# Optimization experiments

Measured on AMD Instinct MI355X. Metric: run time of the kernel, lower is better.

Reference implementation:

```python
import jax, jax.numpy as jnp
import numpy as np

B, D, C, N = 256, 512, 345, 50000
K = 5
ALPHA = 1.0
EPS = 1e-12


def setup_inputs() -> dict:
    key = jax.random.key(0)
    k1, k2, k3, k4, k5 = jax.random.split(key, 5)
    return {
        "features": jax.random.normal(k1, (B, D), dtype=jnp.float32),
        "predictions": jax.random.normal(k2, (B, C), dtype=jnp.float32),
        "fea_bank": jax.random.normal(k3, (N, D), dtype=jnp.float32),
        "score_bank": jax.random.uniform(k4, (N, C), dtype=jnp.float32, minval=1e-3, maxval=1.0),
        "trg_idx": jax.random.randint(k5, (B,), 0, N, dtype=jnp.int64),
    }


def reference(features, predictions, fea_bank, score_bank, trg_idx):
    softmax_out = jax.nn.softmax(predictions, axis=1)  # [B, C]

    # --- no_grad block: bank update + neighbor retrieval ---
    f_norm = features / jnp.maximum(
        jnp.linalg.norm(features, axis=1, keepdims=True), EPS
    )
    f_ng = jax.lax.stop_gradient(f_norm)
    s_ng = jax.lax.stop_gradient(softmax_out)
    fb = fea_bank.at[trg_idx].set(f_ng)       # [N, D]
    sb = score_bank.at[trg_idx].set(s_ng)     # [N, C]
    distance = f_ng @ fb.T                    # [B, N] cosine similarity
    _, idx_near = jax.lax.top_k(distance, K + 1)
    idx_near = idx_near[:, 1:]                # drop self -> [B, K]
    score_near = sb[idx_near]                 # [B, K, C]

    # F.kl_div(input=softmax_out (NOT log), target=score_near):
    # target * (log(target) - input), summed over C and K, mean over B.
    kl = score_near * (jnp.log(score_near) - softmax_out[:, None, :])
    loss = jnp.mean(kl.sum(-1).sum(-1))

    # dispersion: masked pairwise dot of softmax outputs (off-diagonal)
    dot = softmax_out @ softmax_out.T         # [B, B]
    mask = 1.0 - jnp.eye(B, dtype=dot.dtype)
    neg_pred = jnp.mean((dot * mask).sum(-1))
    loss = loss + ALPHA * neg_pred
    return loss
```

## Files before the change

kernel.cpp:

```cpp
#include <hip/hip_runtime.h>
#include <cstdint>

#define BB 256
#define DD 512
#define CC 345
#define NBANK 50000
#define NPAD 50048
#define KNEI 5
#define ALPHAC 1.0f
#define EPSN 1e-12f
#define NHALF 782
#define CSLOTS (NHALF * 2)

typedef short short8 __attribute__((ext_vector_type(8)));
typedef float f32x4 __attribute__((ext_vector_type(4)));
typedef unsigned long long u64;

__device__ inline uint32_t f2bf1(float x) {
    union { float f; uint32_t u; } v; v.f = x;
    return (v.u + 0x7FFFu + ((v.u >> 16) & 1u)) >> 16;
}
__device__ inline uint32_t pack2(float a, float b) {
    return f2bf1(a) | (f2bf1(b) << 16);
}
__device__ inline float bl(uint32_t x) {
    union { uint32_t u; float f; } v; v.u = x << 16; return v.f;
}
__device__ inline float bh(uint32_t x) {
    union { uint32_t u; float f; } v; v.u = x & 0xFFFF0000u; return v.f;
}
__device__ inline u64 mkkey(float v, int j) {
    union { float f; uint32_t u; } c; c.f = v;
    uint32_t b = c.u;
    uint32_t k = (b & 0x80000000u) ? ~b : (b | 0x80000000u);
    return ((u64)k << 32) | (uint32_t)(~j);
}
__device__ inline u64 umax64(u64 a, u64 b) { return a > b ? a : b; }
__device__ inline u64 shfl_xor_u64(u64 v, int m) {
    int lo = __shfl_xor((int)(uint32_t)v, m, 64);
    int hi = __shfl_xor((int)(v >> 32), m, 64);
    return ((u64)(uint32_t)hi << 32) | (uint32_t)lo;
}
__device__ inline void ins6u(u64 k, u64* lv) {
    if (k > lv[5]) {
        int q = 5;
        while (q > 0 && k > lv[q - 1]) { lv[q] = lv[q - 1]; q--; }
        lv[q] = k;
    }
}
__device__ inline void tree6u(u64* sv, int t, const u64* lv) {
#pragma unroll
    for (int r = 0; r < 6; r++) sv[t * 6 + r] = lv[r];
    __syncthreads();
    for (int s = 128; s > 0; s >>= 1) {
        if (t < s) {
            u64 av[6], bv[6], rv[6];
#pragma unroll
            for (int r = 0; r < 6; r++) { av[r] = sv[t * 6 + r]; bv[r] = sv[(t + s) * 6 + r]; }
            int x = 0, y = 0;
#pragma unroll
            for (int o = 0; o < 6; o++) {
                bool pk = av[x] > bv[y];
                rv[o] = pk ? av[x] : bv[y];
                x += pk; y += !pk;
            }
#pragma unroll
            for (int r = 0; r < 6; r++) sv[t * 6 + r] = rv[r];
        }
        __syncthreads();
    }
}
__device__ inline void async16(const void* g, void* l) {
    __builtin_amdgcn_global_load_lds(
        (const __attribute__((address_space(1))) unsigned int*)g,
        (__attribute__((address_space(3))) unsigned int*)l, 16, 0, 0);
}
__device__ inline size_t sw_off(int tile, int r, int ch) {
    return (size_t)tile * 8192 + r * 64 + ((ch ^ (r & 7)) * 8);
}

__global__ void repl_init_kernel(int* __restrict__ repl) {
    int idx = blockIdx.x * 256 + threadIdx.x;
    if (idx < NPAD) repl[idx] = -1;
}

__global__ void winner_kernel(const int* __restrict__ trg, int* __restrict__ repl,
                              float* __restrict__ out) {
    int t = threadIdx.x;
    __shared__ int st[BB];
    if (t == 0) out[0] = 0.f;
    st[t] = trg[t];
    __syncthreads();
    int mv = st[t];
    int w = 1;
    for (int b2 = t + 1; b2 < BB; b2++)
        if (st[b2] == mv) w = 0;
    if (w) repl[mv] = t;
}

__global__ void norm_softmax_kernel(const float* __restrict__ feat,
                                    const float* __restrict__ pred,
                                    unsigned short* __restrict__ fnb,
                                    unsigned short* __restrict__ fnb2,
                                    float* __restrict__ p) {
    int b = blockIdx.x, t = threadIdx.x;
    __shared__ float red[256];
    float x0 = feat[b * DD + t];
    float x1 = feat[b * DD + t + 256];
    red[t] = x0 * x0 + x1 * x1;
    __syncthreads();
    for (int s = 128; s > 0; s >>= 1) {
        if (t < s) red[t] += red[t + s];
        __syncthreads();
    }
    float inv = 1.0f / fmaxf(sqrtf(red[0]), EPSN);
    if (t < 64) {
        const f32x4* src = (const f32x4*)(feat + b * DD + t * 8);
        f32x4 f0 = src[0], f1 = src[1];
        uint4 u = make_uint4(pack2(f0[0] * inv, f0[1] * inv),
                             pack2(f0[2] * inv, f0[3] * inv),
                             pack2(f1[0] * inv, f1[1] * inv),
                             pack2(f1[2] * inv, f1[3] * inv));
        *(uint4*)(fnb + b * DD + t * 8) = u;
        int mtile = b >> 7, r = b & 127, kt = t >> 3, ch = t & 7;
        *(uint4*)(fnb2 + sw_off(mtile * 8 + kt, r, ch)) = u;
    }
    __syncthreads();
    float y0 = (t < CC) ? pred[b * CC + t] : -3.0e38f;
    float y1 = (t + 256 < CC) ? pred[b * CC + t + 256] : -3.0e38f;
    red[t] = fmaxf(y0, y1);
    __syncthreads();
    for (int s = 128; s > 0; s >>= 1) {
        if (t < s) red[t] = fmaxf(red[t], red[t + s]);
        __syncthreads();
    }
    float M = red[0];
    __syncthreads();
    float e0 = (t < CC) ? expf(y0 - M) : 0.f;
    float e1 = (t + 256 < CC) ? expf(y1 - M) : 0.f;
    red[t] = e0 + e1;
    __syncthreads();
    for (int s = 128; s > 0; s >>= 1) {
        if (t < s) red[t] += red[t + s];
        __syncthreads();
    }
    float si = 1.0f / red[0];
    if (t < CC) p[b * CC + t] = e0 * si;
    if (t + 256 < CC) p[b * CC + t + 256] = e1 * si;
}

__global__ __launch_bounds__(256) void gemm_topk_kernel(
        const unsigned short* __restrict__ fnb2, const float* __restrict__ bank,
        const unsigned short* __restrict__ fnb, const int* __restrict__ repl,
        u64* __restrict__ cand) {
    __shared__ __align__(16) char smem[40960];
    unsigned short* As = (unsigned short*)smem;
    unsigned short* Bs = (unsigned short*)(smem + 32768);

    int t = threadIdx.x;
    int ntb = blockIdx.x;
    int j0 = ntb * 64;
    int w = t >> 6, lane = t & 63, quad = lane >> 4, l16 = lane & 15;

    int br = t >> 2, cq = t & 3;
    int bj = j0 + br;
    int rp = (bj < NBANK) ? repl[bj] : -2;

    f32x4 acc[4][4];
#pragma unroll
    for (int mt = 0; mt < 4; mt++)
#pragma unroll
        for (int nt = 0; nt < 4; nt++)
            acc[mt][nt] = (f32x4){0.f, 0.f, 0.f, 0.f};

    const char* fnb2b = (const char*)fnb2;

    for (int kt = 0; kt < 8; kt++) {
        const char* asrc = fnb2b + (size_t)((w < 2 ? kt : kt + 8) * 16384 + (w & 1) * 8192);
        char* adst = smem + w * 8192;
#pragma unroll
        for (int u = 0; u < 8; u++)
            async16(asrc + u * 1024 + lane * 16, adst + u * 1024);
        {
            uint4 b0, b1;
            if (rp >= 0) {
                const uint4* s = (const uint4*)(fnb + (size_t)rp * DD + kt * 64 + cq * 16);
                b0 = s[0]; b1 = s[1];
            } else if (rp == -1) {
                const f32x4* s = (const f32x4*)(bank + (size_t)bj * DD + kt * 64 + cq * 16);
                f32x4 f0 = s[0], f1 = s[1], f2 = s[2], f3 = s[3];
                b0 = make_uint4(pack2(f0[0], f0[1]), pack2(f0[2], f0[3]),
                                pack2(f1[0], f1[1]), pack2(f1[2], f1[3]));
                b1 = make_uint4(pack2(f2[0], f2[1]), pack2(f2[2], f2[3]),
                                pack2(f3[0], f3[1]), pack2(f3[2], f3[3]));
            } else {
                b0 = make_uint4(0, 0, 0, 0);
                b1 = make_uint4(0, 0, 0, 0);
            }
            int c0 = cq * 2;
            *(uint4*)(Bs + br * 64 + ((c0 ^ (br & 7)) * 8)) = b0;
            *(uint4*)(Bs + br * 64 + (((c0 + 1) ^ (br & 7)) * 8)) = b1;
        }
        __syncthreads();
#pragma unroll
        for (int ks = 0; ks < 2; ks++) {
            int swz = ((ks * 4 + quad) ^ (l16 & 7)) * 8;
            short8 af[4], bf[4];
#pragma unroll
            for (int mt = 0; mt < 4; mt++)
                af[mt] = *(const short8*)(As + (w * 64 + mt * 16 + l16) * 64 + swz);
#pragma unroll
            for (int nt = 0; nt < 4; nt++)
                bf[nt] = *(const short8*)(Bs + (nt * 16 + l16) * 64 + swz);
#pragma unroll
            for (int mt = 0; mt < 4; mt++)
#pragma unroll
                for (int nt = 0; nt < 4; nt++)
                    acc[mt][nt] = __builtin_amdgcn_mfma_f32_16x16x32_bf16(
                        af[mt], bf[nt], acc[mt][nt], 0, 0, 0);
        }
        __syncthreads();
    }

    bool maskPad[4];
#pragma unroll
    for (int nt = 0; nt < 4; nt++)
        maskPad[nt] = (ntb == NHALF - 1) && ((j0 + nt * 16 + l16) >= NBANK);

#pragma unroll
    for (int mt = 0; mt < 4; mt++)
#pragma unroll
        for (int r2 = 0; r2 < 4; r2++) {
            u64 k[4];
#pragma unroll
            for (int nt = 0; nt < 4; nt++) {
                int j = j0 + nt * 16 + l16;
                k[nt] = maskPad[nt] ? 0ull : mkkey(acc[mt][nt][r2], j);
            }
            u64 m = umax64(umax64(k[0], k[1]), umax64(k[2], k[3]));
#pragma unroll
            for (int off = 1; off < 16; off <<= 1)
                m = umax64(m, shfl_xor_u64(m, off));
            u64 top1 = m;
#pragma unroll
            for (int nt = 0; nt < 4; nt++) k[nt] = (k[nt] == top1) ? 0ull : k[nt];
            m = umax64(umax64(k[0], k[1]), umax64(k[2], k[3]));
#pragma unroll
            for (int off = 1; off < 16; off <<= 1)
                m = umax64(m, shfl_xor_u64(m, off));
            if (l16 == 0) {
                int gi = w * 64 + mt * 16 + quad * 4 + r2;
                u64* cp = cand + (size_t)gi * CSLOTS + ntb * 2;
                cp[0] = top1; cp[1] = m;
            }
        }
}

__global__ __launch_bounds__(256) void merge_kernel(
        const u64* __restrict__ cand, const unsigned short* __restrict__ fnb,
        const float* __restrict__ bank, const int* __restrict__ repl,
        int* __restrict__ nidx) {
    int i = blockIdx.x, t = threadIdx.x;
    __shared__ u64 sv[1536];
    __shared__ uint32_t fm[25];
    __shared__ int fl[128];
    __shared__ int nf;
    __shared__ float a[512];
    const u64* cr = cand + (size_t)i * CSLOTS;

    u64 lv[6] = {0, 0, 0, 0, 0, 0};
    for (int q = t; q < CSLOTS; q += 256) ins6u(cr[q], lv);
    if (t < 25) fm[t] = 0;
    if (t == 0) nf = 0;
    tree6u(sv, t, lv);
    u64 M6 = sv[5];
    __syncthreads();
    for (int h = t; h < NHALF; h += 256) {
        if (cr[h * 2 + 1] >= M6) {
            int s = atomicAdd(&nf, 1);
            if (s < 128) fl[s] = h;
            atomicOr(&fm[h >> 5], 1u << (h & 31));
        }
    }
    __syncthreads();
    if (nf > 0) {
        uint32_t wrd = ((const uint32_t*)(fnb + (size_t)i * DD))[t];
        a[2 * t] = bl(wrd);
        a[2 * t + 1] = bh(wrd);
        __syncthreads();
        u64 l2[6] = {0, 0, 0, 0, 0, 0};
        for (int q = t; q < CSLOTS; q += 256) {
            int h = q >> 1;
            if (!((fm[h >> 5] >> (h & 31)) & 1u)) ins6u(cr[q], l2);
        }
        int nfl = nf < 128 ? nf : 128;
        for (int s = 0; s < nfl; s++) {
            int h = fl[s];
            if (t < 64) {
                int j = h * 64 + t;
                if (j < NBANK) {
                    int rp = repl[j];
                    float dot = 0.f;
                    if (rp >= 0) {
                        const uint32_t* rw = (const uint32_t*)(fnb + (size_t)rp * DD);
                        for (int kk = 0; kk < 256; kk++) {
                            uint32_t u = rw[kk];
                            dot += bl(u) * a[2 * kk] + bh(u) * a[2 * kk + 1];
                        }
                    } else {
                        const float* rw = bank + (size_t)j * DD;
                        for (int kk = 0; kk < DD; kk++)
                            dot += bl(f2bf1(rw[kk])) * a[kk];
                    }
                    ins6u(mkkey(dot, j), l2);
                }
            }
        }
        __syncthreads();
        tree6u(sv, t, l2);
    }
    if (t == 0) {
#pragma unroll
        for (int r = 1; r < 6; r++)
            nidx[i * KNEI + r - 1] = (int)(~(uint32_t)(sv[r] & 0xFFFFFFFFull));
    }
}

__global__ void kl_negpred_kernel(const float* __restrict__ p,
                                  const float* __restrict__ sbank,
                                  const int* __restrict__ nidx,
                                  const int* __restrict__ trg,
                                  float* __restrict__ out) {
    int bid = blockIdx.x, t = threadIdx.x;
    __shared__ float red[256];
    __shared__ float aux[256];
    if (bid < BB) {
        int b = bid;
        __shared__ int st[BB];
        __shared__ int sj[KNEI], sb[KNEI];
        st[t] = trg[t];
        __syncthreads();
        if (t < KNEI) {
            int j = nidx[b * KNEI + t];
            sj[t] = j;
            int src = -1;
            for (int b2 = 0; b2 < BB; b2++)
                if (st[b2] == j) src = b2;
            sb[t] = src;
        }
        __syncthreads();
        float local = 0.f;
        for (int k = 0; k < KNEI; k++) {
            int j = sj[k], src = sb[k];
            const float* srow = (src >= 0) ? (p + src * CC) : (sbank + (size_t)j * CC);
            for (int c = t; c < CC; c += 256) {
                float s = srow[c];
                local += s * (logf(s) - p[b * CC + c]);
            }
        }
        red[t] = local;
        __syncthreads();
        for (int s = 128; s > 0; s >>= 1) {
            if (t < s) red[t] += red[t + s];
            __syncthreads();
        }
        if (t == 0) atomicAdd(out, red[0] * (1.0f / BB));
    } else {
        int c = bid - BB;
        float v = p[t * CC + c];
        red[t] = v;
        aux[t] = v * v;
        __syncthreads();
        for (int s = 128; s > 0; s >>= 1) {
            if (t < s) { red[t] += red[t + s]; aux[t] += aux[t + s]; }
            __syncthreads();
        }
        if (t == 0) atomicAdd(out, ALPHAC * (red[0] * red[0] - aux[0]) * (1.0f / BB));
    }
}

extern "C" void kernel_launch(void* const* d_in, const int* in_sizes, int n_in,
                              void* d_out, int out_size, void* d_ws, size_t ws_size,
                              hipStream_t stream) {
    const float* feat  = (const float*)d_in[0];
    const float* pred  = (const float*)d_in[1];
    const float* bank  = (const float*)d_in[2];
    const float* sbank = (const float*)d_in[3];
    const int*   trg   = (const int*)d_in[4];
    float* out = (float*)d_out;

    char* ws = (char*)d_ws;
    unsigned short* fnb2 = (unsigned short*)ws;
    unsigned short* fnb  = (unsigned short*)(ws + 262144);
    float*          p    = (float*)(ws + 524288);
    int*            repl = (int*)(ws + 877568);
    u64*            cand = (u64*)(ws + 1077760);
    int*            nidx = (int*)(ws + 4280832);

    repl_init_kernel<<<(NPAD + 255) / 256, 256, 0, stream>>>(repl);
    winner_kernel<<<1, 256, 0, stream>>>(trg, repl, out);
    norm_softmax_kernel<<<BB, 256, 0, stream>>>(feat, pred, fnb, fnb2, p);
    gemm_topk_kernel<<<NHALF, 256, 0, stream>>>(fnb2, bank, fnb, repl, cand);
    merge_kernel<<<BB, 256, 0, stream>>>(cand, fnb, bank, repl, nidx);
    kl_negpred_kernel<<<BB + CC, 256, 0, stream>>>(p, sbank, nidx, trg, out);
}
```

Baseline: 278.5 us.

## Double-buffer LDS tiles and prefetch bank rows in GEMM-topk kernel

Splits shared memory into two stages in the similarity GEMM kernel. The next K-slice's A tile is copied asynchronously and the next bank row is loaded into registers while MFMAs run on the current slice. The B tile is converted and stored after compute, which removes one barrier per iteration and hides global load latency. The cost is doubled LDS per block (about 80KB), which may cut the number of resident blocks per CU, plus extra registers for the prefetched data.

```diff
diff --git a/kernel.cpp b/kernel.cpp
--- a/kernel.cpp
+++ b/kernel.cpp
@@ -153,9 +153,7 @@
         const unsigned short* __restrict__ fnb2, const float* __restrict__ bank,
         const unsigned short* __restrict__ fnb, const int* __restrict__ repl,
         u64* __restrict__ cand) {
-    __shared__ __align__(16) char smem[40960];
-    unsigned short* As = (unsigned short*)smem;
-    unsigned short* Bs = (unsigned short*)(smem + 32768);
+    __shared__ __align__(16) char smem[2][40960];
 
     int t = threadIdx.x;
     int ntb = blockIdx.x;
@@ -165,6 +163,9 @@
     int br = t >> 2, cq = t & 3;
     int bj = j0 + br;
     int rp = (bj < NBANK) ? repl[bj] : -2;
+    const uint4* fsrc = (const uint4*)(fnb + (size_t)((rp >= 0) ? rp : 0) * DD) + cq * 2;
+    const f32x4* bsrc = (const f32x4*)(bank + (size_t)bj * DD) + cq * 4;
+    const char* fnb2b = (const char*)fnb2;
 
     f32x4 acc[4][4];
 #pragma unroll
@@ -173,35 +174,50 @@
         for (int nt = 0; nt < 4; nt++)
             acc[mt][nt] = (f32x4){0.f, 0.f, 0.f, 0.f};
 
-    const char* fnb2b = (const char*)fnb2;
-
-    for (int kt = 0; kt < 8; kt++) {
-        const char* asrc = fnb2b + (size_t)((w < 2 ? kt : kt + 8) * 16384 + (w & 1) * 8192);
-        char* adst = smem + w * 8192;
+    uint4 pb0, pb1;
+    f32x4 pf0, pf1, pf2, pf3;
+
+    if (rp >= 0)       { pb0 = fsrc[0]; pb1 = fsrc[1]; }
+    else if (rp == -1) { pf0 = bsrc[0]; pf1 = bsrc[1]; pf2 = bsrc[2]; pf3 = bsrc[3]; }
+    {
+        const char* asrc = fnb2b + (size_t)((w < 2 ? 0 : 8) * 16384 + (w & 1) * 8192);
+        char* adst = smem[0] + w * 8192;
 #pragma unroll
         for (int u = 0; u < 8; u++)
             async16(asrc + u * 1024 + lane * 16, adst + u * 1024);
-        {
-            uint4 b0, b1;
-            if (rp >= 0) {
-                const uint4* s = (const uint4*)(fnb + (size_t)rp * DD + kt * 64 + cq * 16);
-                b0 = s[0]; b1 = s[1];
-            } else if (rp == -1) {
-                const f32x4* s = (const f32x4*)(bank + (size_t)bj * DD + kt * 64 + cq * 16);
-                f32x4 f0 = s[0], f1 = s[1], f2 = s[2], f3 = s[3];
-                b0 = make_uint4(pack2(f0[0], f0[1]), pack2(f0[2], f0[3]),
-                                pack2(f1[0], f1[1]), pack2(f1[2], f1[3]));
-                b1 = make_uint4(pack2(f2[0], f2[1]), pack2(f2[2], f2[3]),
-                                pack2(f3[0], f3[1]), pack2(f3[2], f3[3]));
-            } else {
-                b0 = make_uint4(0, 0, 0, 0);
-                b1 = make_uint4(0, 0, 0, 0);
-            }
-            int c0 = cq * 2;
-            *(uint4*)(Bs + br * 64 + ((c0 ^ (br & 7)) * 8)) = b0;
-            *(uint4*)(Bs + br * 64 + (((c0 + 1) ^ (br & 7)) * 8)) = b1;
-        }
-        __syncthreads();
+    }
+    {
+        uint4 b0, b1;
+        if (rp >= 0)       { b0 = pb0; b1 = pb1; }
+        else if (rp == -1) {
+            b0 = make_uint4(pack2(pf0[0], pf0[1]), pack2(pf0[2], pf0[3]),
+                            pack2(pf1[0], pf1[1]), pack2(pf1[2], pf1[3]));
+            b1 = make_uint4(pack2(pf2[0], pf2[1]), pack2(pf2[2], pf2[3]),
+                            pack2(pf3[0], pf3[1]), pack2(pf3[2], pf3[3]));
+        } else { b0 = make_uint4(0, 0, 0, 0); b1 = make_uint4(0, 0, 0, 0); }
+        unsigned short* Bs0 = (unsigned short*)(smem[0] + 32768);
+        int c0 = cq * 2;
+        *(uint4*)(Bs0 + br * 64 + ((c0 ^ (br & 7)) * 8)) = b0;
+        *(uint4*)(Bs0 + br * 64 + (((c0 + 1) ^ (br & 7)) * 8)) = b1;
+    }
+    __syncthreads();
+
+    for (int kt = 0; kt < 8; kt++) {
+        int cur = kt & 1;
+        int nxt = cur ^ 1;
+        if (kt < 7) {
+            if (rp >= 0)       { pb0 = fsrc[(kt + 1) * 8];  pb1 = fsrc[(kt + 1) * 8 + 1]; }
+            else if (rp == -1) { pf0 = bsrc[(kt + 1) * 16];     pf1 = bsrc[(kt + 1) * 16 + 1];
+                                 pf2 = bsrc[(kt + 1) * 16 + 2]; pf3 = bsrc[(kt + 1) * 16 + 3]; }
+            const char* asrc = fnb2b +
+                (size_t)((w < 2 ? kt + 1 : kt + 9) * 16384 + (w & 1) * 8192);
+            char* adst = smem[nxt] + w * 8192;
+#pragma unroll
+            for (int u = 0; u < 8; u++)
+                async16(asrc + u * 1024 + lane * 16, adst + u * 1024);
+        }
+        unsigned short* As = (unsigned short*)smem[cur];
+        unsigned short* Bs = (unsigned short*)(smem[cur] + 32768);
 #pragma unroll
         for (int ks = 0; ks < 2; ks++) {
             int swz = ((ks * 4 + quad) ^ (l16 & 7)) * 8;
@@ -218,6 +234,20 @@
                 for (int nt = 0; nt < 4; nt++)
                     acc[mt][nt] = __builtin_amdgcn_mfma_f32_16x16x32_bf16(
                         af[mt], bf[nt], acc[mt][nt], 0, 0, 0);
+        }
+        if (kt < 7) {
+            uint4 b0, b1;
+            if (rp >= 0)       { b0 = pb0; b1 = pb1; }
+            else if (rp == -1) {
+                b0 = make_uint4(pack2(pf0[0], pf0[1]), pack2(pf0[2], pf0[3]),
+                                pack2(pf1[0], pf1[1]), pack2(pf1[2], pf1[3]));
+                b1 = make_uint4(pack2(pf2[0], pf2[1]), pack2(pf2[2], pf2[3]),
+                                pack2(pf3[0], pf3[1]), pack2(pf3[2], pf3[3]));
+            } else { b0 = make_uint4(0, 0, 0, 0); b1 = make_uint4(0, 0, 0, 0); }
+            unsigned short* Bn = (unsigned short*)(smem[nxt] + 32768);
+            int c0 = cq * 2;
+            *(uint4*)(Bn + br * 64 + ((c0 ^ (br & 7)) * 8)) = b0;
+            *(uint4*)(Bn + br * 64 + (((c0 + 1) ^ (br & 7)) * 8)) = b1;
         }
         __syncthreads();
     }
```

Result: no change. 279.8 us (+0.5%).

## Stage whole bank tile in LDS once, read A from global, fuse small kernels

Applied to the files above, without the earlier changes.

The GEMM/top-k kernel now loads the full 64-row bank tile (all 512 dims, converted to bf16 and swizzled) into 64KB of LDS up front. It then runs the MFMA loop without per-k-step barriers, reading the query fragments directly from the global normalized-feature buffer instead of async-copying a pre-swizzled A layout into LDS. The repl init is folded into the norm/softmax kernel, and the merge kernel is fused with the KL and dispersion reduction, which drops the extra pre-swizzled buffer and two launches. The larger LDS footprint lowers occupancy, and A reads now depend on L1/L2 hits.

```diff
diff --git a/kernel.cpp b/kernel.cpp
--- a/kernel.cpp
+++ b/kernel.cpp
@@ -70,40 +70,15 @@
         __syncthreads();
     }
 }
-__device__ inline void async16(const void* g, void* l) {
-    __builtin_amdgcn_global_load_lds(
-        (const __attribute__((address_space(1))) unsigned int*)g,
-        (__attribute__((address_space(3))) unsigned int*)l, 16, 0, 0);
-}
-__device__ inline size_t sw_off(int tile, int r, int ch) {
-    return (size_t)tile * 8192 + r * 64 + ((ch ^ (r & 7)) * 8);
-}
-
-__global__ void repl_init_kernel(int* __restrict__ repl) {
-    int idx = blockIdx.x * 256 + threadIdx.x;
-    if (idx < NPAD) repl[idx] = -1;
-}
-
-__global__ void winner_kernel(const int* __restrict__ trg, int* __restrict__ repl,
-                              float* __restrict__ out) {
-    int t = threadIdx.x;
-    __shared__ int st[BB];
-    if (t == 0) out[0] = 0.f;
-    st[t] = trg[t];
-    __syncthreads();
-    int mv = st[t];
-    int w = 1;
-    for (int b2 = t + 1; b2 < BB; b2++)
-        if (st[b2] == mv) w = 0;
-    if (w) repl[mv] = t;
-}
 
 __global__ void norm_softmax_kernel(const float* __restrict__ feat,
                                     const float* __restrict__ pred,
                                     unsigned short* __restrict__ fnb,
-                                    unsigned short* __restrict__ fnb2,
-                                    float* __restrict__ p) {
+                                    float* __restrict__ p,
+                                    int* __restrict__ repl) {
     int b = blockIdx.x, t = threadIdx.x;
+    int gi = b * 256 + t;
+    if (gi < NPAD) repl[gi] = -1;
     __shared__ float red[256];
     float x0 = feat[b * DD + t];
     float x1 = feat[b * DD + t + 256];
@@ -122,8 +97,6 @@
                              pack2(f1[0] * inv, f1[1] * inv),
                              pack2(f1[2] * inv, f1[3] * inv));
         *(uint4*)(fnb + b * DD + t * 8) = u;
-        int mtile = b >> 7, r = b & 127, kt = t >> 3, ch = t & 7;
-        *(uint4*)(fnb2 + sw_off(mtile * 8 + kt, r, ch)) = u;
     }
     __syncthreads();
     float y0 = (t < CC) ? pred[b * CC + t] : -3.0e38f;
@@ -149,22 +122,52 @@
     if (t + 256 < CC) p[b * CC + t + 256] = e1 * si;
 }
 
+__global__ void winner_kernel(const int* __restrict__ trg, int* __restrict__ repl,
+                              float* __restrict__ out) {
+    int t = threadIdx.x;
+    __shared__ int st[BB];
+    if (t == 0) out[0] = 0.f;
+    st[t] = trg[t];
+    __syncthreads();
+    int mv = st[t];
+    int w = 1;
+    for (int b2 = t + 1; b2 < BB; b2++)
+        if (st[b2] == mv) w = 0;
+    if (w) repl[mv] = t;
+}
+
 __global__ __launch_bounds__(256) void gemm_topk_kernel(
-        const unsigned short* __restrict__ fnb2, const float* __restrict__ bank,
-        const unsigned short* __restrict__ fnb, const int* __restrict__ repl,
-        u64* __restrict__ cand) {
-    __shared__ __align__(16) char smem[40960];
-    unsigned short* As = (unsigned short*)smem;
-    unsigned short* Bs = (unsigned short*)(smem + 32768);
+        const unsigned short* __restrict__ fnb, const float* __restrict__ bank,
+        const int* __restrict__ repl, u64* __restrict__ cand) {
+    __shared__ __align__(16) char smem[65536];
 
     int t = threadIdx.x;
     int ntb = blockIdx.x;
     int j0 = ntb * 64;
     int w = t >> 6, lane = t & 63, quad = lane >> 4, l16 = lane & 15;
 
-    int br = t >> 2, cq = t & 3;
-    int bj = j0 + br;
-    int rp = (bj < NBANK) ? repl[bj] : -2;
+    int rpv = (j0 + lane < NBANK) ? repl[j0 + lane] : -2;
+
+    const char* bankb = (const char*)bank;
+    const char* fnbb = (const char*)fnb;
+
+#pragma unroll 4
+    for (int i = 0; i < 16; i++) {
+        int r = i * 4 + w;
+        int rp = __shfl(rpv, r);
+        uint4 u = make_uint4(0u, 0u, 0u, 0u);
+        if (rp >= 0) {
+            u = *(const uint4*)(fnbb + (size_t)rp * 1024 + lane * 16);
+        } else if (rp == -1) {
+            const f32x4* s = (const f32x4*)(bankb + (size_t)(j0 + r) * 2048 + lane * 32);
+            f32x4 a = s[0], b2 = s[1];
+            u = make_uint4(pack2(a[0], a[1]), pack2(a[2], a[3]),
+                           pack2(b2[0], b2[1]), pack2(b2[2], b2[3]));
+        }
+        int slot = lane ^ (r & 7);
+        *(uint4*)(smem + (size_t)r * 1024 + slot * 16) = u;
+    }
+    __syncthreads();
 
     f32x4 acc[4][4];
 #pragma unroll
@@ -173,45 +176,20 @@
         for (int nt = 0; nt < 4; nt++)
             acc[mt][nt] = (f32x4){0.f, 0.f, 0.f, 0.f};
 
-    const char* fnb2b = (const char*)fnb2;
-
+#pragma unroll
     for (int kt = 0; kt < 8; kt++) {
-        const char* asrc = fnb2b + (size_t)((w < 2 ? kt : kt + 8) * 16384 + (w & 1) * 8192);
-        char* adst = smem + w * 8192;
-#pragma unroll
-        for (int u = 0; u < 8; u++)
-            async16(asrc + u * 1024 + lane * 16, adst + u * 1024);
-        {
-            uint4 b0, b1;
-            if (rp >= 0) {
-                const uint4* s = (const uint4*)(fnb + (size_t)rp * DD + kt * 64 + cq * 16);
-                b0 = s[0]; b1 = s[1];
-            } else if (rp == -1) {
-                const f32x4* s = (const f32x4*)(bank + (size_t)bj * DD + kt * 64 + cq * 16);
-                f32x4 f0 = s[0], f1 = s[1], f2 = s[2], f3 = s[3];
-                b0 = make_uint4(pack2(f0[0], f0[1]), pack2(f0[2], f0[3]),
-                                pack2(f1[0], f1[1]), pack2(f1[2], f1[3]));
-                b1 = make_uint4(pack2(f2[0], f2[1]), pack2(f2[2], f2[3]),
-                                pack2(f3[0], f3[1]), pack2(f3[2], f3[3]));
-            } else {
-                b0 = make_uint4(0, 0, 0, 0);
-                b1 = make_uint4(0, 0, 0, 0);
-            }
-            int c0 = cq * 2;
-            *(uint4*)(Bs + br * 64 + ((c0 ^ (br & 7)) * 8)) = b0;
-            *(uint4*)(Bs + br * 64 + (((c0 + 1) ^ (br & 7)) * 8)) = b1;
-        }
-        __syncthreads();
 #pragma unroll
         for (int ks = 0; ks < 2; ks++) {
-            int swz = ((ks * 4 + quad) ^ (l16 & 7)) * 8;
+            int c = kt * 8 + ks * 4 + quad;
+            int sw = (c ^ (l16 & 7)) * 16;
             short8 af[4], bf[4];
 #pragma unroll
             for (int mt = 0; mt < 4; mt++)
-                af[mt] = *(const short8*)(As + (w * 64 + mt * 16 + l16) * 64 + swz);
+                af[mt] = *(const short8*)(fnbb +
+                    (size_t)(w * 64 + mt * 16 + l16) * 1024 + c * 16);
 #pragma unroll
             for (int nt = 0; nt < 4; nt++)
-                bf[nt] = *(const short8*)(Bs + (nt * 16 + l16) * 64 + swz);
+                bf[nt] = *(const short8*)(smem + (size_t)(nt * 16 + l16) * 1024 + sw);
 #pragma unroll
             for (int mt = 0; mt < 4; mt++)
 #pragma unroll
@@ -219,7 +197,6 @@
                     acc[mt][nt] = __builtin_amdgcn_mfma_f32_16x16x32_bf16(
                         af[mt], bf[nt], acc[mt][nt], 0, 0, 0);
         }
-        __syncthreads();
     }
 
     bool maskPad[4];
@@ -256,11 +233,28 @@
         }
 }
 
-__global__ __launch_bounds__(256) void merge_kernel(
+__global__ __launch_bounds__(256) void mergekl_kernel(
         const u64* __restrict__ cand, const unsigned short* __restrict__ fnb,
         const float* __restrict__ bank, const int* __restrict__ repl,
-        int* __restrict__ nidx) {
-    int i = blockIdx.x, t = threadIdx.x;
+        const float* __restrict__ p, const float* __restrict__ sbank,
+        const int* __restrict__ trg, float* __restrict__ out) {
+    int bid = blockIdx.x, t = threadIdx.x;
+    __shared__ float red[256];
+    if (bid >= BB) {
+        __shared__ float aux[256];
+        int c = bid - BB;
+        float v = p[t * CC + c];
+        red[t] = v;
+        aux[t] = v * v;
+        __syncthreads();
+        for (int s = 128; s > 0; s >>= 1) {
+            if (t < s) { red[t] += red[t + s]; aux[t] += aux[t + s]; }
+            __syncthreads();
+        }
+        if (t == 0) atomicAdd(out, ALPHAC * (red[0] * red[0] - aux[0]) * (1.0f / BB));
+        return;
+    }
+    int i = bid;
     __shared__ u64 sv[1536];
     __shared__ uint32_t fm[25];
     __shared__ int fl[128];
@@ -319,64 +313,34 @@
         __syncthreads();
         tree6u(sv, t, l2);
     }
-    if (t == 0) {
-#pragma unroll
-        for (int r = 1; r < 6; r++)
-            nidx[i * KNEI + r - 1] = (int)(~(uint32_t)(sv[r] & 0xFFFFFFFFull));
-    }
-}
-
-__global__ void kl_negpred_kernel(const float* __restrict__ p,
-                                  const float* __restrict__ sbank,
-                                  const int* __restrict__ nidx,
-                                  const int* __restrict__ trg,
-                                  float* __restrict__ out) {
-    int bid = blockIdx.x, t = threadIdx.x;
-    __shared__ float red[256];
-    __shared__ float aux[256];
-    if (bid < BB) {
-        int b = bid;
-        __shared__ int st[BB];
-        __shared__ int sj[KNEI], sb[KNEI];
-        st[t] = trg[t];
-        __syncthreads();
-        if (t < KNEI) {
-            int j = nidx[b * KNEI + t];
-            sj[t] = j;
-            int src = -1;
-            for (int b2 = 0; b2 < BB; b2++)
-                if (st[b2] == j) src = b2;
-            sb[t] = src;
-        }
-        __syncthreads();
-        float local = 0.f;
-        for (int k = 0; k < KNEI; k++) {
-            int j = sj[k], src = sb[k];
-            const float* srow = (src >= 0) ? (p + src * CC) : (sbank + (size_t)j * CC);
-            for (int c = t; c < CC; c += 256) {
-                float s = srow[c];
-                local += s * (logf(s) - p[b * CC + c]);
-            }
-        }
-        red[t] = local;
-        __syncthreads();
-        for (int s = 128; s > 0; s >>= 1) {
-            if (t < s) red[t] += red[t + s];
-            __syncthreads();
-        }
-        if (t == 0) atomicAdd(out, red[0] * (1.0f / BB));
-    } else {
-        int c = bid - BB;
-        float v = p[t * CC + c];
-        red[t] = v;
-        aux[t] = v * v;
-        __syncthreads();
-        for (int s = 128; s > 0; s >>= 1) {
-            if (t < s) { red[t] += red[t + s]; aux[t] += aux[t + s]; }
-            __syncthreads();
-        }
-        if (t == 0) atomicAdd(out, ALPHAC * (red[0] * red[0] - aux[0]) * (1.0f / BB));
-    }
+    __shared__ int st[BB];
+    __shared__ int sj[KNEI], sb2[KNEI];
+    st[t] = trg[t];
+    if (t < KNEI) {
+        sj[t] = (int)(~(uint32_t)(sv[t + 1] & 0xFFFFFFFFull));
+        sb2[t] = -1;
+    }
+    __syncthreads();
+#pragma unroll
+    for (int k = 0; k < KNEI; k++)
+        if (st[t] == sj[k]) atomicMax(&sb2[k], t);
+    __syncthreads();
+    float local = 0.f;
+    for (int k = 0; k < KNEI; k++) {
+        int j = sj[k], src = sb2[k];
+        const float* srow = (src >= 0) ? (p + src * CC) : (sbank + (size_t)j * CC);
+        for (int c = t; c < CC; c += 256) {
+            float s = srow[c];
+            local += s * (logf(s) - p[i * CC + c]);
+        }
+    }
+    red[t] = local;
+    __syncthreads();
+    for (int s = 128; s > 0; s >>= 1) {
+        if (t < s) red[t] += red[t + s];
+        __syncthreads();
+    }
+    if (t == 0) atomicAdd(out, red[0] * (1.0f / BB));
 }
 
 extern "C" void kernel_launch(void* const* d_in, const int* in_sizes, int n_in,
@@ -390,17 +354,13 @@
     float* out = (float*)d_out;
 
     char* ws = (char*)d_ws;
-    unsigned short* fnb2 = (unsigned short*)ws;
-    unsigned short* fnb  = (unsigned short*)(ws + 262144);
-    float*          p    = (float*)(ws + 524288);
-    int*            repl = (int*)(ws + 877568);
-    u64*            cand = (u64*)(ws + 1077760);
-    int*            nidx = (int*)(ws + 4280832);
-
-    repl_init_kernel<<<(NPAD + 255) / 256, 256, 0, stream>>>(repl);
+    unsigned short* fnb  = (unsigned short*)ws;
+    float*          p    = (float*)(ws + 262144);
+    int*            repl = (int*)(ws + 615424);
+    u64*            cand = (u64*)(ws + 815616);
+
+    norm_softmax_kernel<<<BB, 256, 0, stream>>>(feat, pred, fnb, p, repl);
     winner_kernel<<<1, 256, 0, stream>>>(trg, repl, out);
-    norm_softmax_kernel<<<BB, 256, 0, stream>>>(feat, pred, fnb, fnb2, p);
-    gemm_topk_kernel<<<NHALF, 256, 0, stream>>>(fnb2, bank, fnb, repl, cand);
-    merge_kernel<<<BB, 256, 0, stream>>>(cand, fnb, bank, repl, nidx);
-    kl_negpred_kernel<<<BB + CC, 256, 0, stream>>>(p, sbank, nidx, trg, out);
-}
+    gemm_topk_kernel<<<NHALF, 256, 0, stream>>>(fnb, bank, repl, cand);
+    mergekl_kernel<<<BB + CC, 256, 0, stream>>>(cand, fnb, bank, repl, p, sbank, trg, out);
+}
```

Measured after the change: 298.7 us. 1.07x slower.
